# Kernel optimization log

Hardware: AMD Instinct MI355X
Metric: run time of the kernel (lower is better)

Reference implementation:

```python
import jax, jax.numpy as jnp
import numpy as np
from jax import lax

NUM_CLASSES = 80
STRIDES = (8, 16, 32, 64, 128)
PRE_NMS_THRESH = 0.05
PRE_NMS_TOPK = 1000
NMS_THRESH = 0.6
POST_NMS_TOPK = 100
NUM_CONVS = 4
CIN = 256
BATCH = 2
FEAT_SHAPES = ((100, 152), (50, 76), (25, 38), (13, 19), (7, 10))
CLASS_OFFSET = 10000.0  # coordinate offset for class-aware NMS


def conv3x3(x, w, b):
    # x: [B,C,H,W], w: [O,C,3,3] -> [B,O,H,W], stride 1, SAME padding
    y = lax.conv_general_dilated(x, w, (1, 1), 'SAME',
                                 dimension_numbers=('NCHW', 'OIHW', 'NCHW'))
    return y + b[None, :, None, None]


def tower(x, Ws, Bs):
    # sequence of (conv3x3 -> ReLU), norm='none'
    for i in range(Ws.shape[0]):
        x = jax.nn.relu(conv3x3(x, Ws[i], Bs[i]))
    return x


def compute_locations(h, w, stride):
    sx = jnp.arange(w, dtype=jnp.float32) * stride
    sy = jnp.arange(h, dtype=jnp.float32) * stride
    yy, xx = jnp.meshgrid(sy, sx, indexing='ij')
    return jnp.stack([xx.reshape(-1), yy.reshape(-1)], axis=1) + stride // 2  # [HW,2]


def nms_single(boxes, scores, classes):
    # boxes [N,4], scores [N] (>=0), classes [N] int. Greedy class-aware NMS.
    off = classes.astype(boxes.dtype) * CLASS_OFFSET
    b = boxes + off[:, None]
    area = (b[:, 2] - b[:, 0]) * (b[:, 3] - b[:, 1])

    def step(s, _):
        i = jnp.argmax(s)
        v = s[i]
        bi = b[i]
        lt = jnp.maximum(bi[:2], b[:, :2])
        rb = jnp.minimum(bi[2:], b[:, 2:])
        wh = jnp.maximum(rb - lt, 0.0)
        inter = wh[:, 0] * wh[:, 1]
        iou = inter / (area[i] + area - inter + 1e-9)
        s2 = jnp.where(iou > NMS_THRESH, -1.0, s).at[i].set(-1.0)
        return s2, (i, v)

    _, (idx, vals) = lax.scan(step, scores, None, length=POST_NMS_TOPK)
    valid = vals > 0.0
    out = jnp.concatenate(
        [boxes[idx], vals[:, None], classes[idx].astype(boxes.dtype)[:, None]], axis=1)
    return jnp.where(valid[:, None], out, 0.0)  # [POST_NMS_TOPK, 6]


def _forward(p3, p4, p5, p6, p7, cls_w, cls_b, box_w, box_b,
             logit_w, logit_b, pred_w, pred_b, ctr_w, ctr_b, scales):
    feats = (p3, p4, p5, p6, p7)
    boxes_all, scores_all, cls_all = [], [], []
    for l, x in enumerate(feats):
        # share_tower has 0 convs -> identity
        ct = tower(x, cls_w, cls_b)
        bt = tower(x, box_w, box_b)
        logits = conv3x3(ct, logit_w, logit_b)                   # [B,C,H,W]
        ctr = conv3x3(bt, ctr_w, ctr_b)                          # [B,1,H,W]
        reg = jax.nn.relu(conv3x3(bt, pred_w, pred_b) * scales[l])  # [B,4,H,W]
        B, _, H, W = logits.shape
        HW = H * W
        locs = compute_locations(H, W, STRIDES[l])               # [HW,2]
        cls_prob = jax.nn.sigmoid(logits).transpose(0, 2, 3, 1).reshape(B, HW, NUM_CLASSES)
        ctr_prob = jax.nn.sigmoid(ctr).reshape(B, HW, 1)
        s = cls_prob * ctr_prob                                  # thresh_with_ctr
        s = jnp.where(s > PRE_NMS_THRESH, s, 0.0)
        k = min(PRE_NMS_TOPK, HW * NUM_CLASSES)
        vals, idx = lax.top_k(s.reshape(B, HW * NUM_CLASSES), k)
        loc_idx = idx // NUM_CLASSES                             # [B,k]
        cls_idx = idx % NUM_CLASSES
        reg_f = reg.transpose(0, 2, 3, 1).reshape(B, HW, 4)
        reg_sel = jnp.take_along_axis(reg_f, loc_idx[..., None], axis=1)  # [B,k,4]
        loc_sel = locs[loc_idx]                                  # [B,k,2]
        boxes = jnp.stack([loc_sel[..., 0] - reg_sel[..., 0],
                           loc_sel[..., 1] - reg_sel[..., 1],
                           loc_sel[..., 0] + reg_sel[..., 2],
                           loc_sel[..., 1] + reg_sel[..., 3]], axis=-1)
        boxes_all.append(boxes)
        scores_all.append(jnp.sqrt(jnp.maximum(vals, 1e-12)))
        cls_all.append(cls_idx)
    boxes = jnp.concatenate(boxes_all, axis=1)    # [B,N,4]
    scores = jnp.concatenate(scores_all, axis=1)  # [B,N]
    classes = jnp.concatenate(cls_all, axis=1)    # [B,N]
    return jax.vmap(nms_single)(boxes, scores, classes)  # [B,POST_NMS_TOPK,6]


def setup_inputs() -> dict:
    key = jax.random.key(0)
    ks = jax.random.split(key, 12)
    std = 0.05  # larger than fcos init std=0.01 so decoded scores exceed the threshold
    inp = {}
    for i, (h, w) in enumerate(FEAT_SHAPES):
        inp[f'p{i + 3}'] = jax.random.normal(ks[i], (BATCH, CIN, h, w), dtype=jnp.float32)
    inp['cls_w'] = jax.random.normal(ks[5], (NUM_CONVS, CIN, CIN, 3, 3), dtype=jnp.float32) * std
    inp['cls_b'] = jnp.zeros((NUM_CONVS, CIN), dtype=jnp.float32)
    inp['box_w'] = jax.random.normal(ks[6], (NUM_CONVS, CIN, CIN, 3, 3), dtype=jnp.float32) * std
    inp['box_b'] = jnp.zeros((NUM_CONVS, CIN), dtype=jnp.float32)
    inp['logit_w'] = jax.random.normal(ks[7], (NUM_CLASSES, CIN, 3, 3), dtype=jnp.float32) * std
    inp['logit_b'] = jnp.zeros((NUM_CLASSES,), dtype=jnp.float32)
    inp['pred_w'] = jax.random.normal(ks[8], (4, CIN, 3, 3), dtype=jnp.float32) * std
    inp['pred_b'] = jnp.zeros((4,), dtype=jnp.float32)
    inp['ctr_w'] = jax.random.normal(ks[9], (1, CIN, 3, 3), dtype=jnp.float32) * std
    inp['ctr_b'] = jnp.zeros((1,), dtype=jnp.float32)
    inp['scales'] = jnp.ones((5,), dtype=jnp.float32)
    return inp


def reference(p3, p4, p5, p6, p7, cls_w, cls_b, box_w, box_b,
              logit_w, logit_b, pred_w, pred_b, ctr_w, ctr_b, scales):
    return _forward(p3, p4, p5, p6, p7, cls_w, cls_b, box_w, box_b,
                    logit_w, logit_b, pred_w, pred_b, ctr_w, ctr_b, scales)
```

## Files before the change

kernel.cpp:

```cpp
#include <hip/hip_runtime.h>
#include <stdint.h>
#include <math.h>

#define NCLS 80
#define TOTHW 20267
#define WLAYER 1179648ull

typedef _Float16 f16x8 __attribute__((ext_vector_type(8)));
typedef float f32x4 __attribute__((ext_vector_type(4)));
typedef short s16x8 __attribute__((ext_vector_type(8)));

static constexpr int cLW[5]    = {152,76,38,19,10};
static constexpr int cLH[5]    = {100,50,25,13,7};
static constexpr int cLHW[5]   = {15200,3800,950,247,70};
static constexpr int cLCUM[5]  = {0,15200,19000,19950,20197};
static constexpr int cLSTR[5]  = {8,16,32,64,128};
static constexpr int cCB[11]   = {0,123,246,278,310,319,328,331,334,335,336};
static constexpr int cPBASE[11]= {0,15744,31488,35584,39680,40832,41984,42368,42752,42880,43008};
static constexpr int cRCUM[11] = {0,100,200,250,300,325,350,363,376,383,390};
static constexpr int cCPX64[6] = {0,475,594,624,632,635};
#define NPXB64 635
#define SBE 11010048ull

__device__ __forceinline__ void split2(float y, unsigned short& h0, unsigned short& h1) {
  _Float16 b0 = (_Float16)y;
  float f0 = (float)b0;
  _Float16 b1 = (_Float16)((y - f0) * 2048.0f);
  h0 = __builtin_bit_cast(unsigned short, b0);
  h1 = __builtin_bit_cast(unsigned short, b1);
}

__device__ __forceinline__ void lds_hist_add(uint32_t* h, uint32_t bucket) {
  unsigned long long act = __ballot(1);
  int lane = (int)(threadIdx.x & 63u);
  int leader = __ffsll(act) - 1;
  uint32_t lb = (uint32_t)__shfl((int)bucket, leader, 64);
  unsigned long long same = __ballot(bucket == lb);
  if (same == act) {
    if (lane == leader) atomicAdd(&h[bucket], (uint32_t)__popcll(act));
  } else {
    atomicAdd(&h[bucket], 1u);
  }
}

__global__ void k_zero(unsigned short* X0, unsigned short* X1) {
  int px = blockIdx.x * 256 + threadIdx.x;
  if (px >= 43008) return;
  int pi = 0;
#pragma unroll
  for (int i = 1; i < 10; i++) if (px >= cPBASE[i]) pi = i;
  const int l = pi >> 1;
  const int p = px - cPBASE[pi];
  const int W = cLW[l], H = cLH[l], PWl = W + 2;
  const int pr = p / PWl, pc = p - pr * PWl;
  if (pr >= 1 && pr <= H && pc >= 1 && pc <= W) return;
  s16x8 z = {0,0,0,0,0,0,0,0};
  size_t base = (size_t)px * 256;
#pragma unroll
  for (int k = 0; k < 32; k++) {
    *reinterpret_cast<s16x8*>(X0 + base + k*8) = z;
    *reinterpret_cast<s16x8*>(X1 + base + k*8) = z;
  }
}

__global__ __launch_bounds__(256)
void k_prep(const float* __restrict__ p0, const float* __restrict__ p1,
            const float* __restrict__ p2, const float* __restrict__ p3,
            const float* __restrict__ p4,
            unsigned short* __restrict__ X0, unsigned short* __restrict__ X1) {
  int bx = blockIdx.x;
  int pi = 0;
#pragma unroll
  for (int i = 1; i < 10; i++) if (bx >= cRCUM[i]) pi = i;
  const int h = bx - cRCUM[pi];
  const int l = pi >> 1, bidx = pi & 1;
  const int W = cLW[l], HW = cLHW[l], PWl = W + 2;
  const int PB = cPBASE[pi];
  const float* src;
  if (l == 0) src = p0; else if (l == 1) src = p1; else if (l == 2) src = p2;
  else if (l == 3) src = p3; else src = p4;
  src += (size_t)bidx * 256 * HW;
  const int tid = threadIdx.x;
  __shared__ float tile[64][152];
  for (int c0 = 0; c0 < 256; c0 += 64) {
    {
      int c = tid >> 2, wq = tid & 3;
      for (int w = wq; w < W; w += 4)
        tile[c][w] = src[(size_t)(c0 + c) * HW + h * W + w];
    }
    __syncthreads();
    {
      int c8 = (tid & 7) * 8;
      for (int w = tid >> 3; w < W; w += 32) {
        size_t base = (size_t)(PB + (h + 1) * PWl + (w + 1)) * 256 + c0 + c8;
        unsigned short a0[8], a1[8];
#pragma unroll
        for (int j = 0; j < 8; j++) split2(tile[c8 + j][w], a0[j], a1[j]);
        *reinterpret_cast<s16x8*>(X0 + base) = *reinterpret_cast<s16x8*>(a0);
        *reinterpret_cast<s16x8*>(X1 + base) = *reinterpret_cast<s16x8*>(a1);
      }
    }
    __syncthreads();
  }
}

__global__ void k_packall(const float* __restrict__ box_w, const float* __restrict__ cls_w,
                          const float* __restrict__ logit_w, unsigned short* __restrict__ wp) {
  const int layer = blockIdx.y;
  const int oc = blockIdx.x, c = threadIdx.x;
  const float* w; int Cout = 256;
  const size_t WSTRIDE = (size_t)256 * 2304;
  if (layer < 4)      w = box_w + (size_t)layer * WSTRIDE;
  else if (layer < 8) w = cls_w + (size_t)(layer - 4) * WSTRIDE;
  else { w = logit_w; Cout = NCLS; }
  if (oc >= Cout) return;
  unsigned short* wpL = wp + (size_t)layer * WLAYER;
#pragma unroll
  for (int r = 0; r < 9; r++) {
    float v = w[((size_t)oc * 256 + c) * 9 + r];
    unsigned short h0, h1;
    split2(v, h0, h1);
    wpL[((size_t)(r * 2 + 0) * 256 + oc) * 256 + c] = h0;
    wpL[((size_t)(r * 2 + 1) * 256 + oc) * 256 + c] = h1;
  }
}

__global__ void k_packhead(const float* __restrict__ ctw, const float* __restrict__ pdw,
                           float* __restrict__ wh) {
  const int r = blockIdx.x, c = threadIdx.x;
  float* d = &wh[((size_t)r * 256 + c) * 5];
  d[0] = ctw[c * 9 + r];
#pragma unroll
  for (int q = 0; q < 4; q++) d[1 + q] = pdw[(size_t)q * 2304 + c * 9 + r];
}

struct MfArgs {
  const unsigned short *X0, *X1;
  const unsigned short *Wp;
  const float* bias;
  unsigned short *Y0, *Y1;
  float* actf;
  float* scores;
  const float* ctrp;
  uint32_t* hist;
};

template<int EPI>
__global__ __launch_bounds__(256, 2)
void conv_mfma(MfArgs a) {
  __shared__ __align__(16) unsigned short lds[18432];
  const int tid = threadIdx.x;
  const int lane = tid & 63;
  const int wid = tid >> 6;

  const int nwg = (EPI == 2) ? 336 : 672;
  const int id = blockIdx.x;
  const int w = (id & 7) * (nwg >> 3) + (id >> 3);
  const int oc0 = (EPI == 2) ? 0 : (w & 1) * 128;
  int bx = (EPI == 2) ? w : (w >> 1);

  int pi = 0;
#pragma unroll
  for (int i = 1; i < 10; i++) if (bx >= cCB[i]) pi = i;
  const int l = pi >> 1, bidx = pi & 1;
  const int pxb = bx - cCB[pi];
  const int px0 = pxb * 128;
  const int PB = cPBASE[pi];
  const int W = cLW[l], H = cLH[l], HW = cLHW[l], PWl = W + 2;

  int row_[2], g_[2];
#pragma unroll
  for (int d = 0; d < 2; d++) {
    int idx2 = tid + d * 256;
    row_[d] = idx2 >> 2;
    g_[d] = idx2 & 3;
  }

  const int wr = wid >> 1, wc = wid & 1;
  const int kg = lane >> 4, ln15 = lane & 15;
  int fA[4], fB[4];
#pragma unroll
  for (int mt = 0; mt < 4; mt++) fA[mt] = (wr * 64 + mt * 16 + ln15) * 72 + kg * 8;
#pragma unroll
  for (int nt = 0; nt < 4; nt++) fB[nt] = 9216 + (wc * 64 + nt * 16 + ln15) * 72 + kg * 8;

  f32x4 acc0[4][4], acc1[4][4];
#pragma unroll
  for (int mt = 0; mt < 4; mt++)
#pragma unroll
    for (int nt = 0; nt < 4; nt++) {
      acc0[mt][nt] = (f32x4){0.f, 0.f, 0.f, 0.f};
      acc1[mt][nt] = (f32x4){0.f, 0.f, 0.f, 0.f};
    }

  s16x8 ra[4], rb[4];
  auto loadstep = [&](int step) {
    const int rr = step >> 3;
    const int c0 = (step & 7) << 5;
    const int dh = rr / 3 - 1, dw = rr - (rr / 3) * 3 - 1;
    const long long OFF = (long long)(PB + px0 + dh * PWl + dw);
#pragma unroll
    for (int s = 0; s < 2; s++) {
      const unsigned short* Xs = (s == 0) ? a.X0 : a.X1;
      const unsigned short* Ws = a.Wp + (size_t)(rr * 2 + s) * 65536;
#pragma unroll
      for (int d = 0; d < 2; d++) {
        ra[s * 2 + d] = *reinterpret_cast<const s16x8*>(Xs + (OFF + row_[d]) * 256 + c0 + g_[d] * 8);
        rb[s * 2 + d] = *reinterpret_cast<const s16x8*>(Ws + (size_t)(oc0 + row_[d]) * 256 + c0 + g_[d] * 8);
      }
    }
  };

  loadstep(0);
  for (int step = 0; step < 72; ++step) {
    if (step) __syncthreads();
#pragma unroll
    for (int s = 0; s < 2; s++)
#pragma unroll
      for (int d = 0; d < 2; d++) {
        const int o = row_[d] * 72 + (s * 4 + g_[d]) * 8;
        *reinterpret_cast<s16x8*>(&lds[o]) = ra[s * 2 + d];
        *reinterpret_cast<s16x8*>(&lds[o + 9216]) = rb[s * 2 + d];
      }
    __syncthreads();
    if (step != 71) loadstep(step + 1);

    f16x8 bv[4][2];
#pragma unroll
    for (int nt = 0; nt < 4; nt++) {
      bv[nt][0] = *reinterpret_cast<const f16x8*>(&lds[fB[nt]]);
      bv[nt][1] = *reinterpret_cast<const f16x8*>(&lds[fB[nt] + 32]);
    }
#pragma unroll
    for (int mt = 0; mt < 4; mt++) {
      f16x8 av0 = *reinterpret_cast<const f16x8*>(&lds[fA[mt]]);
      f16x8 av1 = *reinterpret_cast<const f16x8*>(&lds[fA[mt] + 32]);
#pragma unroll
      for (int nt = 0; nt < 4; nt++) {
        acc0[mt][nt] = __builtin_amdgcn_mfma_f32_16x16x32_f16(av0, bv[nt][0], acc0[mt][nt], 0, 0, 0);
        acc1[mt][nt] = __builtin_amdgcn_mfma_f32_16x16x32_f16(av0, bv[nt][1], acc1[mt][nt], 0, 0, 0);
        acc1[mt][nt] = __builtin_amdgcn_mfma_f32_16x16x32_f16(av1, bv[nt][0], acc1[mt][nt], 0, 0, 0);
      }
    }
  }
  __syncthreads();

  uint32_t* hh = nullptr;
  if (EPI == 2) {
    hh = reinterpret_cast<uint32_t*>(lds);
    for (int i = tid; i < 4096; i += 256) hh[i] = 0;
    __syncthreads();
  }
#pragma unroll
  for (int mt = 0; mt < 4; mt++) {
#pragma unroll
    for (int i = 0; i < 4; i++) {
      const int pxl = wr * 64 + mt * 16 + (lane >> 4) * 4 + i;
      const int p = px0 + pxl;
      const int pr = p / PWl, pc = p - pr * PWl;
      if (!(pr >= 1 && pr <= H && pc >= 1 && pc <= W)) continue;
      const int hw = (pr - 1) * W + (pc - 1);
#pragma unroll
      for (int nt = 0; nt < 4; nt++) {
        const int oc = oc0 + wc * 64 + nt * 16 + ln15;
        const float v = acc0[mt][nt][i] + acc1[mt][nt][i] * 4.8828125e-4f;
        if (EPI == 2) {
          if (oc < NCLS) {
            float y = v + a.bias[oc];
            float pcs = 1.0f / (1.0f + expf(-y));
            float s = pcs * a.ctrp[2 * cLCUM[l] + bidx * HW + hw];
            s = (s > 0.05f) ? s : 0.f;
            a.scores[(size_t)NCLS * (2 * cLCUM[l] + bidx * HW) + (size_t)oc * HW + hw] = s;
            lds_hist_add(hh, __float_as_uint(s) >> 20);
          }
        } else {
          float y = fmaxf(v + a.bias[oc], 0.f);
          if (EPI == 0) {
            size_t o = (size_t)(PB + p) * 256 + oc;
            unsigned short h0, h1;
            split2(y, h0, h1);
            a.Y0[o] = h0; a.Y1[o] = h1;
          } else {
            a.actf[(size_t)(PB + p) * 256 + oc] = y;
          }
        }
      }
    }
  }
  if (EPI == 2) {
    __syncthreads();
    uint32_t* gh = a.hist + (size_t)(l * 2 + bidx) * 4096;
    for (int i = tid; i < 4096; i += 256) { uint32_t v = hh[i]; if (v) atomicAdd(&gh[i], v); }
  }
}

__global__ __launch_bounds__(256)
void k_head2(const float* __restrict__ headact, const float* __restrict__ wh,
             const float* __restrict__ ctb, const float* __restrict__ pdb,
             const float* __restrict__ scl,
             float* __restrict__ ctrp, float* __restrict__ regb) {
  __shared__ float swh[11520];
  for (int i = threadIdx.x; i < 11520; i += 256) swh[i] = wh[i];
  int bx = blockIdx.x; int l = 0;
#pragma unroll
  for (int i = 1; i < 5; i++) if (bx >= cCPX64[i]) l = i;
  const int lblk = bx - cCPX64[l];
  const int H = cLH[l], W = cLW[l], HW = cLHW[l]; const int N = 2 * HW;
  const int lane = threadIdx.x & 63;
  const int wv = threadIdx.x >> 6;
  __syncthreads();
  const float bb0 = ctb[0], bb1 = pdb[0], bb2 = pdb[1], bb3 = pdb[2], bb4 = pdb[3];
  const float sc = scl[l];
  const int c4 = lane * 4;
  for (int t = 0; t < 16; ++t) {
    int px = lblk * 64 + wv * 16 + t;
    if (px >= N) break;
    int bb = px / HW; int hw = px - bb * HW; int hh = hw / W; int ww = hw - hh * W;
    const int PB = cPBASE[l * 2 + bb];
    float a0 = 0.f, a1 = 0.f, a2 = 0.f, a3 = 0.f, a4 = 0.f;
#pragma unroll
    for (int r = 0; r < 9; r++) {
      int dh = r / 3 - 1, dw = r % 3 - 1;
      int ih = hh + dh, iw = ww + dw;
      if (!(((unsigned)ih < (unsigned)H) && ((unsigned)iw < (unsigned)W))) continue;
      const float4 x = *reinterpret_cast<const float4*>(
          headact + (size_t)(PB + (ih + 1) * (W + 2) + (iw + 1)) * 256 + c4);
      const float* wr = &swh[(size_t)(r * 256 + c4) * 5];
      a0 = fmaf(x.x, wr[0],  a0); a1 = fmaf(x.x, wr[1],  a1); a2 = fmaf(x.x, wr[2],  a2);
      a3 = fmaf(x.x, wr[3],  a3); a4 = fmaf(x.x, wr[4],  a4);
      a0 = fmaf(x.y, wr[5],  a0); a1 = fmaf(x.y, wr[6],  a1); a2 = fmaf(x.y, wr[7],  a2);
      a3 = fmaf(x.y, wr[8],  a3); a4 = fmaf(x.y, wr[9],  a4);
      a0 = fmaf(x.z, wr[10], a0); a1 = fmaf(x.z, wr[11], a1); a2 = fmaf(x.z, wr[12], a2);
      a3 = fmaf(x.z, wr[13], a3); a4 = fmaf(x.z, wr[14], a4);
      a0 = fmaf(x.w, wr[15], a0); a1 = fmaf(x.w, wr[16], a1); a2 = fmaf(x.w, wr[17], a2);
      a3 = fmaf(x.w, wr[18], a3); a4 = fmaf(x.w, wr[19], a4);
    }
#pragma unroll
    for (int off = 32; off > 0; off >>= 1) {
      a0 += __shfl_xor(a0, off, 64); a1 += __shfl_xor(a1, off, 64); a2 += __shfl_xor(a2, off, 64);
      a3 += __shfl_xor(a3, off, 64); a4 += __shfl_xor(a4, off, 64);
    }
    if (lane == 0) {
      const int gi = 2 * cLCUM[l] + bb * HW + hw;
      ctrp[gi] = 1.0f / (1.0f + expf(-(a0 + bb0)));
      float* rg = regb + (size_t)gi * 4;
      rg[0] = fmaxf((a1 + bb1) * sc, 0.f);
      rg[1] = fmaxf((a2 + bb2) * sc, 0.f);
      rg[2] = fmaxf((a3 + bb3) * sc, 0.f);
      rg[3] = fmaxf((a4 + bb4) * sc, 0.f);
    }
  }
}

__global__ void k_init(uint32_t* __restrict__ hist, uint32_t* __restrict__ ctrA,
                       uint32_t* __restrict__ ctrB, uint32_t* __restrict__ survCnt) {
  int i = blockIdx.x * blockDim.x + threadIdx.x;
  if (i < 40960) hist[i] = 0;
  if (i < 10) { ctrA[i] = 0; ctrB[i] = 0; }
  if (i < 2) survCnt[i] = 0;
}

__global__ __launch_bounds__(256)
void k_select(const uint32_t* __restrict__ hist, int* __restrict__ meta) {
  const int sid = blockIdx.x;
  const uint32_t* gh = hist + (size_t)sid * 4096;
  __shared__ uint32_t ps[256];
  uint32_t sum = 0;
  for (int i = 0; i < 16; i++) sum += gh[threadIdx.x * 16 + i];
  ps[threadIdx.x] = sum;
  __syncthreads();
  if (threadIdx.x == 0) {
    uint32_t c = 0; int T = 0, m = 1000;
    for (int ch = 255; ch >= 0; --ch) {
      if (c + ps[ch] >= 1000u) {
        for (int t = ch * 16 + 15; t >= ch * 16; --t) {
          uint32_t hv = gh[t];
          if (c + hv >= 1000u) { T = t; m = (int)(1000u - c); break; }
          c += hv;
        }
        break;
      }
      c += ps[ch];
    }
    meta[sid * 4 + 0] = T;
    meta[sid * 4 + 1] = (int)c;
    meta[sid * 4 + 2] = m;
    meta[sid * 4 + 3] = (int)gh[T];
  }
}

__global__ __launch_bounds__(256)
void k_collect(const float* __restrict__ scores, const int* __restrict__ meta,
               unsigned long long* __restrict__ listA, unsigned long long* __restrict__ listB,
               uint32_t* __restrict__ ctrA, uint32_t* __restrict__ ctrB) {
  const int sid = blockIdx.y; const int l = sid >> 1, b = sid & 1;
  const int HW = cLHW[l]; const int size = NCLS * HW;
  const int base = blockIdx.x * 4096;
  if (base >= size) return;
  const size_t sbase = (size_t)NCLS * (2 * cLCUM[l] + b * HW);
  const float* sb = scores + sbase;
  unsigned long long* lB = listB + sbase;
  unsigned long long* lA = listA + (size_t)sid * 1024;
  const uint32_t T = (uint32_t)meta[sid * 4];
  const int lane = (int)(threadIdx.x & 63u);
  __shared__ uint32_t cA, cB, bA, bB;
  if (threadIdx.x == 0) { cA = 0; cB = 0; }
  __syncthreads();
  uint32_t wa = 0, wb = 0;
  for (int j = 0; j < 16; j++) {
    int i = base + threadIdx.x + j * 256;
    bool inb = (i < size);
    uint32_t bits = inb ? __float_as_uint(sb[i]) : 0u;
    uint32_t bkt = bits >> 20;
    unsigned long long mA = __ballot(inb && bkt > T);
    unsigned long long mB = __ballot(inb && bkt == T);
    if (lane == 0) { wa += (uint32_t)__popcll(mA); wb += (uint32_t)__popcll(mB); }
  }
  if (lane == 0) { if (wa) atomicAdd(&cA, wa); if (wb) atomicAdd(&cB, wb); }
  __syncthreads();
  if (threadIdx.x == 0) {
    bA = cA ? atomicAdd(&ctrA[sid], cA) : 0u;
    bB = cB ? atomicAdd(&ctrB[sid], cB) : 0u;
    cA = 0; cB = 0;
  }
  __syncthreads();
  for (int j = 0; j < 16; j++) {
    int i = base + threadIdx.x + j * 256;
    bool inb = (i < size);
    uint32_t bits = inb ? __float_as_uint(sb[i]) : 0u;
    uint32_t bkt = bits >> 20;
    bool pA = inb && bkt > T;
    bool pB = inb && bkt == T;
    unsigned long long key = 0;
    if (pA || pB) {
      int cls = i / HW; int hw = i - cls * HW;
      uint32_t idx = (uint32_t)(hw * NCLS + cls);
      key = ((unsigned long long)bits << 32) | (unsigned long long)(0xFFFFFFFFu - idx);
    }
    unsigned long long mA = __ballot(pA);
    unsigned long long mB = __ballot(pB);
    unsigned long long lt = (1ull << lane) - 1ull;
    if (mA) {
      int ld = __ffsll(mA) - 1;
      uint32_t wbs = 0;
      if (lane == ld) wbs = atomicAdd(&cA, (uint32_t)__popcll(mA));
      wbs = (uint32_t)__shfl((int)wbs, ld, 64);
      if (pA) {
        uint32_t pos = bA + wbs + (uint32_t)__popcll(mA & lt);
        if (pos < 1024u) lA[pos] = key;
      }
    }
    if (mB) {
      int ld = __ffsll(mB) - 1;
      uint32_t wbs = 0;
      if (lane == ld) wbs = atomicAdd(&cB, (uint32_t)__popcll(mB));
      wbs = (uint32_t)__shfl((int)wbs, ld, 64);
      if (pB) lB[bB + wbs + (uint32_t)__popcll(mB & lt)] = key;
    }
  }
}

__global__ __launch_bounds__(1024)
void k_refine(const int* __restrict__ meta, const unsigned long long* __restrict__ listB,
              unsigned long long* __restrict__ listA, uint32_t* __restrict__ ctrA) {
  const int sid = blockIdx.x; const int l = sid >> 1, b = sid & 1;
  const int HW = cLHW[l];
  const size_t sbase = (size_t)NCLS * (2 * cLCUM[l] + b * HW);
  const unsigned long long* lB = listB + sbase;
  const int nB = meta[sid * 4 + 3];
  int m = meta[sid * 4 + 2];
  __shared__ uint32_t h[256];
  __shared__ unsigned long long sPre;
  __shared__ int sM;
  __shared__ uint32_t sCnt;
  unsigned long long prefix = 0, mask = 0;
  for (int p = 7; p >= 0; --p) {
    for (int i = threadIdx.x; i < 256; i += 1024) h[i] = 0;
    __syncthreads();
    for (int i = threadIdx.x; i < nB; i += 1024) {
      unsigned long long k = lB[i];
      if ((k & mask) == prefix) {
        uint32_t bkt = (uint32_t)((k >> (p * 8)) & 255ull);
        lds_hist_add(h, bkt);
      }
    }
    __syncthreads();
    if (threadIdx.x == 0) {
      uint32_t c = 0; int sel = 0; int mnew = m;
      for (int t = 255; t >= 0; --t) {
        if (c + h[t] >= (uint32_t)m) { sel = t; mnew = m - (int)c; break; }
        c += h[t];
      }
      sPre = prefix | ((unsigned long long)sel << (p * 8));
      sM = mnew;
    }
    __syncthreads();
    prefix = sPre; m = sM;
    mask |= (0xFFull << (p * 8));
    __syncthreads();
  }
  if (threadIdx.x == 0) sCnt = ctrA[sid];
  __syncthreads();
  for (int i = threadIdx.x; i < nB; i += 1024) {
    unsigned long long k = lB[i];
    if (k >= prefix) {
      uint32_t pos = atomicAdd(&sCnt, 1u);
      if (pos < 1024u) listA[(size_t)sid * 1024 + pos] = k;
    }
  }
  __syncthreads();
  if (threadIdx.x == 0) ctrA[sid] = sCnt;
}

__global__ __launch_bounds__(256)
void k_sortdec(const unsigned long long* __restrict__ listA, const uint32_t* __restrict__ ctrA,
               const float* __restrict__ regb, float* __restrict__ cbox,
               float* __restrict__ cscr, float* __restrict__ ccls) {
  const int sid = blockIdx.x; const int l = sid >> 1, b = sid & 1;
  const int HW = cLHW[l], W = cLW[l];
  __shared__ unsigned long long key[1024];
  int n = (int)ctrA[sid]; if (n > 1024) n = 1024;
  for (int i = threadIdx.x; i < 1024; i += 256)
    key[i] = (i < n) ? listA[(size_t)sid * 1024 + i] : 0ull;
  __syncthreads();
  for (int len = 2; len <= 1024; len <<= 1) {
    for (int j = len >> 1; j > 0; j >>= 1) {
      for (int t = threadIdx.x; t < 512; t += 256) {
        int i = ((t & ~(j - 1)) << 1) | (t & (j - 1));
        int pp = i | j;
        unsigned long long a = key[i], bq = key[pp];
        bool desc = ((i & len) == 0);
        if ((a < bq) == desc) { key[i] = bq; key[pp] = a; }
      }
      __syncthreads();
    }
  }
  for (int r = threadIdx.x; r < 1000; r += 256) {
    unsigned long long k = key[r];
    uint32_t bits = (uint32_t)(k >> 32);
    uint32_t idx = 0xFFFFFFFFu - (uint32_t)(k & 0xFFFFFFFFull);
    float val = __uint_as_float(bits);
    float sc = sqrtf(fmaxf(val, 1e-12f));
    int cls = (int)(idx % NCLS); int loc = (int)(idx / NCLS);
    int hh = loc / W; int ww = loc - hh * W;
    float cx = (float)(ww * cLSTR[l] + (cLSTR[l] >> 1));
    float cy = (float)(hh * cLSTR[l] + (cLSTR[l] >> 1));
    const float* rg = regb + (size_t)(2 * cLCUM[l] + b * HW + loc) * 4;
    int slot = b * 5000 + l * 1000 + r;
    cbox[slot * 4 + 0] = cx - rg[0];
    cbox[slot * 4 + 1] = cy - rg[1];
    cbox[slot * 4 + 2] = cx + rg[2];
    cbox[slot * 4 + 3] = cy + rg[3];
    cscr[slot] = sc;
    ccls[slot] = (float)cls;
  }
}

#define NMSC 1536
__global__ __launch_bounds__(256)
void k_nmscls(const float* __restrict__ cbox, const float* __restrict__ cscr,
              const float* __restrict__ ccls,
              unsigned long long* __restrict__ surv, uint32_t* __restrict__ survCnt) {
  const int cls = blockIdx.x;
  const int b = blockIdx.y;
  __shared__ unsigned short mslot[5024];
  __shared__ float ms[5024];
  __shared__ float kx1[NMSC], ky1[NMSC], kx2[NMSC], ky2[NMSC], kar[NMSC];
  __shared__ uint32_t mcnt;
  __shared__ int sPick; __shared__ float sPickV;
  __shared__ float pb[5];
  __shared__ float wvv[4]; __shared__ int wvi[4];
  if (threadIdx.x == 0) mcnt = 0;
  __syncthreads();
  const float fc = (float)cls;
  for (int j = threadIdx.x; j < 5000; j += 256) {
    if (ccls[b * 5000 + j] == fc) {
      uint32_t p = atomicAdd(&mcnt, 1u);
      mslot[p] = (unsigned short)j;
      ms[p] = cscr[b * 5000 + j];
    }
  }
  __syncthreads();
  const int n = (int)mcnt;
  if (n == 0) return;
  const float off = fc * 10000.0f;
  const int nc = n < NMSC ? n : NMSC;
  for (int i = threadIdx.x; i < nc; i += 256) {
    const float4 bq = *reinterpret_cast<const float4*>(cbox + ((size_t)b * 5000 + mslot[i]) * 4);
    float x1 = bq.x + off, y1 = bq.y + off, x2 = bq.z + off, y2 = bq.w + off;
    kx1[i] = x1; ky1[i] = y1; kx2[i] = x2; ky2[i] = y2; kar[i] = (x2 - x1) * (y2 - y1);
  }
  __syncthreads();
  const int lane = threadIdx.x & 63, wv = threadIdx.x >> 6;
  for (int it = 0; it < 100; ++it) {
    float best = -1.f; int bi = 0x7FFF; int bidx = 0;
    for (int i = threadIdx.x; i < n; i += 256) {
      float v = ms[i];
      int sl = mslot[i];
      if (v > best || (v == best && sl < bi)) { best = v; bi = sl; bidx = i; }
    }
    for (int o = 32; o > 0; o >>= 1) {
      float ov = __shfl_down(best, o, 64);
      int oi = __shfl_down(bi, o, 64);
      int ox = __shfl_down(bidx, o, 64);
      if (ov > best || (ov == best && oi < bi)) { best = ov; bi = oi; bidx = ox; }
    }
    if (lane == 0) { wvv[wv] = best; wvi[wv] = (bidx << 13) | bi; }
    __syncthreads();
    if (threadIdx.x == 0) {
      float bb = wvv[0]; int pk = wvi[0];
      for (int q = 1; q < 4; q++) {
        float v = wvv[q]; int c = wvi[q];
        if (v > bb || (v == bb && (c & 8191) < (pk & 8191))) { bb = v; pk = c; }
      }
      sPickV = bb; sPick = pk;
      if (bb >= 0.f) {
        int slot = pk & 8191;
        uint32_t bits = __float_as_uint(bb);
        uint32_t gslot = (uint32_t)(b * 5000 + slot);
        unsigned long long key = ((unsigned long long)bits << 32) |
                                 (unsigned long long)(0xFFFFFFFFu - gslot);
        uint32_t pos = atomicAdd(&survCnt[b], 1u);
        surv[(size_t)b * 5000 + pos] = key;
        const float4 bx = *reinterpret_cast<const float4*>(cbox + (size_t)gslot * 4);
        pb[0] = bx.x + off; pb[1] = bx.y + off; pb[2] = bx.z + off; pb[3] = bx.w + off;
        pb[4] = (pb[2] - pb[0]) * (pb[3] - pb[1]);
      }
    }
    __syncthreads();
    if (sPickV < 0.f) break;
    const int pidx = sPick >> 13;
    const float bx1 = pb[0], by1 = pb[1], bx2 = pb[2], by2 = pb[3], ba = pb[4];
    for (int i = threadIdx.x; i < n; i += 256) {
      float v = ms[i];
      if (v < 0.f) continue;
      float x1, y1, x2, y2, ar;
      if (i < NMSC) {
        x1 = kx1[i]; y1 = ky1[i]; x2 = kx2[i]; y2 = ky2[i]; ar = kar[i];
      } else {
        const float4 bq = *reinterpret_cast<const float4*>(cbox + ((size_t)b * 5000 + mslot[i]) * 4);
        x1 = bq.x + off; y1 = bq.y + off; x2 = bq.z + off; y2 = bq.w + off;
        ar = (x2 - x1) * (y2 - y1);
      }
      float ix1 = fmaxf(bx1, x1), iy1 = fmaxf(by1, y1);
      float ix2 = fminf(bx2, x2), iy2 = fminf(by2, y2);
      float iw = fmaxf(ix2 - ix1, 0.f), ih = fmaxf(iy2 - iy1, 0.f);
      float inter = iw * ih;
      float iou = inter / ((ba + ar - inter) + 1e-9f);
      if (iou > 0.6f || i == pidx) ms[i] = -1.0f;
    }
    __syncthreads();
  }
}

__global__ __launch_bounds__(1024)
void k_nmsfinal(const unsigned long long* __restrict__ surv, const uint32_t* __restrict__ survCnt,
                const float* __restrict__ cbox, const float* __restrict__ ccls,
                float* __restrict__ out) {
  const int b = blockIdx.x;
  const int n = (int)survCnt[b];
  const unsigned long long* sv = surv + (size_t)b * 5000;
  const int m = n < 100 ? n : 100;
  __shared__ uint32_t h[256];
  __shared__ unsigned long long sPre; __shared__ int sM;
  __shared__ unsigned long long topk[128];
  __shared__ uint32_t tcnt;
  unsigned long long prefix = 0, mask = 0;
  int mm = m;
  if (m > 0) {
    for (int p = 7; p >= 0; --p) {
      for (int i = threadIdx.x; i < 256; i += 1024) h[i] = 0;
      __syncthreads();
      for (int i = threadIdx.x; i < n; i += 1024) {
        unsigned long long k = sv[i];
        if ((k & mask) == prefix) lds_hist_add(h, (uint32_t)((k >> (p * 8)) & 255ull));
      }
      __syncthreads();
      if (threadIdx.x == 0) {
        uint32_t c = 0; int sel = 0; int mnew = mm;
        for (int t = 255; t >= 0; --t) {
          if (c + h[t] >= (uint32_t)mm) { sel = t; mnew = mm - (int)c; break; }
          c += h[t];
        }
        sPre = prefix | ((unsigned long long)sel << (p * 8));
        sM = mnew;
      }
      __syncthreads();
      prefix = sPre; mm = sM;
      mask |= (0xFFull << (p * 8));
      __syncthreads();
    }
  }
  if (threadIdx.x == 0) tcnt = 0;
  for (int i = threadIdx.x; i < 128; i += 1024) topk[i] = 0;
  __syncthreads();
  if (m > 0) {
    for (int i = threadIdx.x; i < n; i += 1024) {
      unsigned long long k = sv[i];
      if (k >= prefix) {
        uint32_t p = atomicAdd(&tcnt, 1u);
        if (p < 128) topk[p] = k;
      }
    }
  }
  __syncthreads();
  for (int len = 2; len <= 128; len <<= 1) {
    for (int j = len >> 1; j > 0; j >>= 1) {
      for (int t = threadIdx.x; t < 64; t += 1024) {
        int i = ((t & ~(j - 1)) << 1) | (t & (j - 1));
        int pp = i | j;
        unsigned long long a = topk[i], bq = topk[pp];
        bool desc = ((i & len) == 0);
        if ((a < bq) == desc) { topk[i] = bq; topk[pp] = a; }
      }
      __syncthreads();
    }
  }
  if (threadIdx.x < 100) {
    int it = threadIdx.x;
    float* orow = out + ((size_t)b * 100 + it) * 6;
    if (it < m) {
      unsigned long long k = topk[it];
      uint32_t gslot = 0xFFFFFFFFu - (uint32_t)(k & 0xFFFFFFFFull);
      const float4 bx = *reinterpret_cast<const float4*>(cbox + (size_t)gslot * 4);
      orow[0] = bx.x; orow[1] = bx.y; orow[2] = bx.z; orow[3] = bx.w;
      orow[4] = __uint_as_float((uint32_t)(k >> 32));
      orow[5] = ccls[gslot];
    } else {
      orow[0] = 0.f; orow[1] = 0.f; orow[2] = 0.f;
      orow[3] = 0.f; orow[4] = 0.f; orow[5] = 0.f;
    }
  }
}

static inline size_t alignup(size_t x) { return (x + 255) & ~(size_t)255; }

extern "C" void kernel_launch(void* const* d_in, const int* in_sizes, int n_in,
                              void* d_out, int out_size, void* d_ws, size_t ws_size,
                              hipStream_t stream) {
  (void)in_sizes; (void)n_in; (void)out_size; (void)ws_size;
  const float* p0 = (const float*)d_in[0];
  const float* p1 = (const float*)d_in[1];
  const float* p2 = (const float*)d_in[2];
  const float* p3 = (const float*)d_in[3];
  const float* p4 = (const float*)d_in[4];
  const float* cls_w   = (const float*)d_in[5];
  const float* cls_b   = (const float*)d_in[6];
  const float* box_w   = (const float*)d_in[7];
  const float* box_b   = (const float*)d_in[8];
  const float* logit_w = (const float*)d_in[9];
  const float* logit_b = (const float*)d_in[10];
  const float* pred_w  = (const float*)d_in[11];
  const float* pred_b  = (const float*)d_in[12];
  const float* ctr_w   = (const float*)d_in[13];
  const float* ctr_b   = (const float*)d_in[14];
  const float* scales  = (const float*)d_in[15];

  char* base = (char*)d_ws;
  size_t off = 0;
  auto take = [&](size_t bytes) { void* p = base + off; off = alignup(off + bytes); return p; };
  float* regb = (float*)take((size_t)4 * 2 * TOTHW * 4);
  float* ctrp = (float*)take((size_t)2 * TOTHW * 4);
  uint32_t* hist = (uint32_t*)take((size_t)40960 * 4);
  int* meta = (int*)take((size_t)40 * 4);
  uint32_t* ctrA = (uint32_t*)take(256);
  uint32_t* ctrB = (uint32_t*)take(256);
  uint32_t* survCnt = (uint32_t*)take(256);
  unsigned long long* listA = (unsigned long long*)take((size_t)10 * 1024 * 8);
  unsigned long long* surv = (unsigned long long*)take((size_t)2 * 5000 * 8);
  float* cbox = (float*)take((size_t)2 * 5000 * 16);
  float* cscr = (float*)take((size_t)2 * 5000 * 4);
  float* ccls = (float*)take((size_t)2 * 5000 * 4);
  float* wh   = (float*)take((size_t)9 * 256 * 5 * 4);
  unsigned short* wpackF = (unsigned short*)take((size_t)9 * WLAYER * 2);
  unsigned short* P_0 = (unsigned short*)take(SBE * 2);
  unsigned short* P_1 = (unsigned short*)take(SBE * 2);
  unsigned short* R1_0 = (unsigned short*)take(SBE * 2);
  unsigned short* R1_1 = (unsigned short*)take(SBE * 2);
  unsigned short* R2_0 = (unsigned short*)take(SBE * 2);
  unsigned short* R2_1 = (unsigned short*)take(SBE * 2);
  (void)take(65536);
  float* scores = (float*)R1_0;
  unsigned long long* listB = (unsigned long long*)R2_0;
  float* headact = (float*)R2_0;

  hipLaunchKernelGGL(k_init, dim3(160), dim3(256), 0, stream, hist, ctrA, ctrB, survCnt);
  hipLaunchKernelGGL(k_packhead, dim3(9), dim3(256), 0, stream, ctr_w, pred_w, wh);
  hipLaunchKernelGGL(k_packall, dim3(256, 9), dim3(256), 0, stream, box_w, cls_w, logit_w, wpackF);
  hipLaunchKernelGGL(k_zero, dim3(168), dim3(256), 0, stream, P_0, P_1);
  hipLaunchKernelGGL(k_zero, dim3(168), dim3(256), 0, stream, R1_0, R1_1);
  hipLaunchKernelGGL(k_zero, dim3(168), dim3(256), 0, stream, R2_0, R2_1);
  hipLaunchKernelGGL(k_prep, dim3(390), dim3(256), 0, stream, p0, p1, p2, p3, p4, P_0, P_1);

  auto runConv = [&](int epi, int layer, const unsigned short* x0, const unsigned short* x1,
                     const float* bias, unsigned short* y0, unsigned short* y1,
                     float* af, float* sc) {
    MfArgs a;
    a.X0 = x0; a.X1 = x1; a.Wp = wpackF + (size_t)layer * WLAYER; a.bias = bias;
    a.Y0 = y0; a.Y1 = y1; a.actf = af; a.scores = sc; a.ctrp = ctrp;
    a.hist = hist;
    if (epi == 0)      hipLaunchKernelGGL(conv_mfma<0>, dim3(672), dim3(256), 0, stream, a);
    else if (epi == 1) hipLaunchKernelGGL(conv_mfma<1>, dim3(672), dim3(256), 0, stream, a);
    else               hipLaunchKernelGGL(conv_mfma<2>, dim3(336), dim3(256), 0, stream, a);
  };

  runConv(0, 0, P_0,  P_1,  box_b + 0,   R1_0, R1_1, nullptr, nullptr);
  runConv(0, 1, R1_0, R1_1, box_b + 256, R2_0, R2_1, nullptr, nullptr);
  runConv(0, 2, R2_0, R2_1, box_b + 512, R1_0, R1_1, nullptr, nullptr);
  runConv(1, 3, R1_0, R1_1, box_b + 768, nullptr, nullptr, headact, nullptr);
  hipLaunchKernelGGL(k_head2, dim3(NPXB64), dim3(256), 0, stream, headact, wh, ctr_b,
                     pred_b, scales, ctrp, regb);
  hipLaunchKernelGGL(k_zero, dim3(168), dim3(256), 0, stream, R2_0, R2_1);

  runConv(0, 4, P_0,  P_1,  cls_b + 0,   R1_0, R1_1, nullptr, nullptr);
  runConv(0, 5, R1_0, R1_1, cls_b + 256, R2_0, R2_1, nullptr, nullptr);
  runConv(0, 6, R2_0, R2_1, cls_b + 512, R1_0, R1_1, nullptr, nullptr);
  runConv(0, 7, R1_0, R1_1, cls_b + 768, R2_0, R2_1, nullptr, nullptr);
  runConv(2, 8, R2_0, R2_1, logit_b, nullptr, nullptr, nullptr, scores);

  hipLaunchKernelGGL(k_select,  dim3(10), dim3(256), 0, stream, hist, meta);
  hipLaunchKernelGGL(k_collect, dim3(297, 10), dim3(256), 0, stream, scores, meta, listA, listB, ctrA, ctrB);
  hipLaunchKernelGGL(k_refine,  dim3(10), dim3(1024), 0, stream, meta, listB, listA, ctrA);
  hipLaunchKernelGGL(k_sortdec, dim3(10), dim3(256), 0, stream, listA, ctrA, regb, cbox, cscr, ccls);
  hipLaunchKernelGGL(k_nmscls,  dim3(NCLS, 2), dim3(256), 0, stream, cbox, cscr, ccls, surv, survCnt);
  hipLaunchKernelGGL(k_nmsfinal, dim3(2), dim3(1024), 0, stream, surv, survCnt, cbox, ccls, (float*)d_out);
}
```

Baseline: 2.180 ms.

## Load MFMA weight fragments directly from global memory and double-buffer activation LDS

```diff
diff --git a/kernel.cpp b/kernel.cpp
--- a/kernel.cpp
+++ b/kernel.cpp
@@ -115,13 +115,16 @@
   else { w = logit_w; Cout = NCLS; }
   if (oc >= Cout) return;
   unsigned short* wpL = wp + (size_t)layer * WLAYER;
+  const int ocf = oc >> 4, ln = oc & 15;
+  const int kc = c >> 5, kg = (c >> 3) & 3, e = c & 7;
+  const int lane = kg * 16 + ln;
 #pragma unroll
   for (int r = 0; r < 9; r++) {
     float v = w[((size_t)oc * 256 + c) * 9 + r];
     unsigned short h0, h1;
     split2(v, h0, h1);
-    wpL[((size_t)(r * 2 + 0) * 256 + oc) * 256 + c] = h0;
-    wpL[((size_t)(r * 2 + 1) * 256 + oc) * 256 + c] = h1;
+    wpL[((((size_t)(r * 2 + 0) * 16 + ocf) * 8 + kc) * 64 + lane) * 8 + e] = h0;
+    wpL[((((size_t)(r * 2 + 1) * 16 + ocf) * 8 + kc) * 64 + lane) * 8 + e] = h1;
   }
 }
 
@@ -178,11 +181,10 @@
 
   const int wr = wid >> 1, wc = wid & 1;
   const int kg = lane >> 4, ln15 = lane & 15;
-  int fA[4], fB[4];
+  int fA[4];
 #pragma unroll
   for (int mt = 0; mt < 4; mt++) fA[mt] = (wr * 64 + mt * 16 + ln15) * 72 + kg * 8;
-#pragma unroll
-  for (int nt = 0; nt < 4; nt++) fB[nt] = 9216 + (wc * 64 + nt * 16 + ln15) * 72 + kg * 8;
+  const int ocfb = (oc0 >> 4) + wc * 4;
 
   f32x4 acc0[4][4], acc1[4][4];
 #pragma unroll
@@ -193,8 +195,8 @@
       acc1[mt][nt] = (f32x4){0.f, 0.f, 0.f, 0.f};
     }
 
-  s16x8 ra[4], rb[4];
-  auto loadstep = [&](int step) {
+  s16x8 ra[4];
+  auto loadA = [&](int step) {
     const int rr = step >> 3;
     const int c0 = (step & 7) << 5;
     const int dh = rr / 3 - 1, dw = rr - (rr / 3) * 3 - 1;
@@ -202,48 +204,62 @@
 #pragma unroll
     for (int s = 0; s < 2; s++) {
       const unsigned short* Xs = (s == 0) ? a.X0 : a.X1;
-      const unsigned short* Ws = a.Wp + (size_t)(rr * 2 + s) * 65536;
+#pragma unroll
+      for (int d = 0; d < 2; d++)
+        ra[s * 2 + d] = *reinterpret_cast<const s16x8*>(Xs + (OFF + row_[d]) * 256 + c0 + g_[d] * 8);
+    }
+  };
+  auto writeA = [&](int buf) {
+#pragma unroll
+    for (int s = 0; s < 2; s++)
 #pragma unroll
       for (int d = 0; d < 2; d++) {
-        ra[s * 2 + d] = *reinterpret_cast<const s16x8*>(Xs + (OFF + row_[d]) * 256 + c0 + g_[d] * 8);
-        rb[s * 2 + d] = *reinterpret_cast<const s16x8*>(Ws + (size_t)(oc0 + row_[d]) * 256 + c0 + g_[d] * 8);
-      }
-    }
+        const int o = buf * 9216 + row_[d] * 72 + (s * 4 + g_[d]) * 8;
+        *reinterpret_cast<s16x8*>(&lds[o]) = ra[s * 2 + d];
+      }
   };
-
-  loadstep(0);
-  for (int step = 0; step < 72; ++step) {
-    if (step) __syncthreads();
-#pragma unroll
-    for (int s = 0; s < 2; s++)
-#pragma unroll
-      for (int d = 0; d < 2; d++) {
-        const int o = row_[d] * 72 + (s * 4 + g_[d]) * 8;
-        *reinterpret_cast<s16x8*>(&lds[o]) = ra[s * 2 + d];
-        *reinterpret_cast<s16x8*>(&lds[o + 9216]) = rb[s * 2 + d];
-      }
-    __syncthreads();
-    if (step != 71) loadstep(step + 1);
-
-    f16x8 bv[4][2];
+  auto loadB = [&](int step, f16x8* bv) {
+    const int rr = step >> 3, cc = step & 7;
 #pragma unroll
     for (int nt = 0; nt < 4; nt++) {
-      bv[nt][0] = *reinterpret_cast<const f16x8*>(&lds[fB[nt]]);
-      bv[nt][1] = *reinterpret_cast<const f16x8*>(&lds[fB[nt] + 32]);
-    }
+      const size_t bo = ((size_t)((rr * 2) * 16 + ocfb + nt) * 8 + cc) * 512 + lane * 8;
+      bv[nt * 2 + 0] = *reinterpret_cast<const f16x8*>(a.Wp + bo);
+      bv[nt * 2 + 1] = *reinterpret_cast<const f16x8*>(a.Wp + bo + 65536);
+    }
+  };
+  auto mfmaStep = [&](int buf, const f16x8* bv) {
+    f16x8 av[4][2];
 #pragma unroll
     for (int mt = 0; mt < 4; mt++) {
-      f16x8 av0 = *reinterpret_cast<const f16x8*>(&lds[fA[mt]]);
-      f16x8 av1 = *reinterpret_cast<const f16x8*>(&lds[fA[mt] + 32]);
+      av[mt][0] = *reinterpret_cast<const f16x8*>(&lds[buf * 9216 + fA[mt]]);
+      av[mt][1] = *reinterpret_cast<const f16x8*>(&lds[buf * 9216 + fA[mt] + 32]);
+    }
+#pragma unroll
+    for (int mt = 0; mt < 4; mt++)
 #pragma unroll
       for (int nt = 0; nt < 4; nt++) {
-        acc0[mt][nt] = __builtin_amdgcn_mfma_f32_16x16x32_f16(av0, bv[nt][0], acc0[mt][nt], 0, 0, 0);
-        acc1[mt][nt] = __builtin_amdgcn_mfma_f32_16x16x32_f16(av0, bv[nt][1], acc1[mt][nt], 0, 0, 0);
-        acc1[mt][nt] = __builtin_amdgcn_mfma_f32_16x16x32_f16(av1, bv[nt][0], acc1[mt][nt], 0, 0, 0);
-      }
-    }
-  }
-  __syncthreads();
+        acc0[mt][nt] = __builtin_amdgcn_mfma_f32_16x16x32_f16(av[mt][0], bv[nt * 2 + 0], acc0[mt][nt], 0, 0, 0);
+        acc1[mt][nt] = __builtin_amdgcn_mfma_f32_16x16x32_f16(av[mt][0], bv[nt * 2 + 1], acc1[mt][nt], 0, 0, 0);
+        acc1[mt][nt] = __builtin_amdgcn_mfma_f32_16x16x32_f16(av[mt][1], bv[nt * 2 + 0], acc1[mt][nt], 0, 0, 0);
+      }
+  };
+
+  f16x8 bv0[8], bv1[8];
+  loadA(0); writeA(0);
+  loadA(1);
+  loadB(0, bv0);
+  __syncthreads();
+
+  for (int sp = 0; sp < 72; sp += 2) {
+    if (sp + 1 < 72) { writeA(1); loadB(sp + 1, bv1); }
+    if (sp + 2 < 72) loadA(sp + 2);
+    mfmaStep(0, bv0);
+    __syncthreads();
+    if (sp + 2 < 72) { writeA(0); loadB(sp + 2, bv0); }
+    if (sp + 3 < 72) loadA(sp + 3);
+    mfmaStep(1, bv1);
+    __syncthreads();
+  }
 
   uint32_t* hh = nullptr;
   if (EPI == 2) {
```

Result: faster. 2.053 ms (-5.8%).
